# Optimization experiments

Hardware: AMD Instinct MI355X
Metric: run time of the kernel (lower is better)

The kernel has to match this reference:

```python
import jax, jax.numpy as jnp
import numpy as np

EMBED_DIM = 1024
N_TOKENS = 8192


def setup_inputs() -> dict:
    key = jax.random.key(0)
    k1, k2, k3 = jax.random.split(key, 3)
    inputs = jax.random.normal(k1, (N_TOKENS, EMBED_DIM), dtype=jnp.float32)
    rotation_params = jax.random.normal(k2, (EMBED_DIM, EMBED_DIM), dtype=jnp.float32)
    entangle_params = jax.random.normal(k3, (EMBED_DIM, EMBED_DIM), dtype=jnp.float32)
    return {"inputs": inputs, "rotation_params": rotation_params, "entangle_params": entangle_params}


def reference(inputs, rotation_params, entangle_params):
    # query/key projections from externally supplied params
    embed_dim = inputs.shape[-1]
    wq = rotation_params.reshape(embed_dim, -1)
    wk = entangle_params.reshape(embed_dim, -1)
    query = inputs @ wq          # [N, d]
    key = inputs @ wk            # [N, d]
    scale = 1.0 / jnp.sqrt(jnp.float32(embed_dim))
    scores = jax.nn.softmax(jnp.einsum('nd,md->nm', query, key) * scale, axis=-1)  # [N, N]
    context = scores @ inputs    # attend over raw inputs (V = inputs)
    return context
```

## Files before the change

kernel.cpp:

```cpp
#include <hip/hip_runtime.h>
#include <hip/hip_bf16.h>


typedef _Float16 f16x8 __attribute__((ext_vector_type(8)));
typedef float    f32x4 __attribute__((ext_vector_type(4)));

__device__ __forceinline__ void g2lds16(const _Float16* g, _Float16* l) {
    __builtin_amdgcn_global_load_lds(
        (__attribute__((address_space(1))) unsigned int*)(g),
        (__attribute__((address_space(3))) unsigned int*)(l),
        16, 0, 0);
}


__global__ void prep_x(const float* __restrict__ src,
                       _Float16* __restrict__ hi, _Float16* __restrict__ lo,
                       _Float16* __restrict__ xt, int R, int C) {
    __shared__ float tile[32][33];
    int c0 = blockIdx.x * 32, r0 = blockIdx.y * 32;
    int tx = threadIdx.x, ty = threadIdx.y;
#pragma unroll
    for (int k = 0; k < 4; ++k) {
        int r = ty + 8 * k;
        size_t idx = (size_t)(r0 + r) * C + c0 + tx;
        float v = src[idx];
        tile[r][tx] = v;
        _Float16 h = (_Float16)v;
        hi[idx] = h;
        lo[idx] = (_Float16)(v - (float)h);
    }
    __syncthreads();
#pragma unroll
    for (int k = 0; k < 4; ++k) {
        float v = tile[tx][ty + 8 * k];
        xt[(size_t)(c0 + ty + 8 * k) * R + r0 + tx] = (_Float16)v;
    }
}

__global__ void transpose_split(const float* __restrict__ src,
                                _Float16* __restrict__ dhi,
                                _Float16* __restrict__ dlo,
                                int R, int C) {
    __shared__ float tile[32][33];
    int c0 = blockIdx.x * 32, r0 = blockIdx.y * 32;
    int tx = threadIdx.x, ty = threadIdx.y;
#pragma unroll
    for (int k = 0; k < 4; ++k)
        tile[ty + 8 * k][tx] = src[(size_t)(r0 + ty + 8 * k) * C + c0 + tx];
    __syncthreads();
#pragma unroll
    for (int k = 0; k < 4; ++k) {
        float v = tile[tx][ty + 8 * k];
        _Float16 h = (_Float16)v;
        size_t idx = (size_t)(c0 + ty + 8 * k) * R + r0 + tx;
        dhi[idx] = h;
        dlo[idx] = (_Float16)(v - (float)h);
    }
}

__global__ __launch_bounds__(256) void add_rows(const float* __restrict__ a,
                                                const float* __restrict__ b,
                                                float* __restrict__ out, long n4) {
    long i = (long)blockIdx.x * blockDim.x + threadIdx.x;
    long stride = (long)gridDim.x * blockDim.x;
    for (; i < n4; i += stride) {
        float4 x = ((const float4*)a)[i];
        float4 y = ((const float4*)b)[i];
        x.x += y.x; x.y += y.y; x.z += y.z; x.w += y.w;
        ((float4*)out)[i] = x;
    }
}

template <int TERMS, int BKH, int SWAP, int SPLIT_OUT>
__global__ __launch_bounds__(512, 2) void gemm_p4(
    const _Float16* __restrict__ Ahi, const _Float16* __restrict__ Alo,
    const _Float16* __restrict__ Bhi, const _Float16* __restrict__ Blo,
    float* __restrict__ C, _Float16* __restrict__ Chi, _Float16* __restrict__ Clo,
    long lda, long ldb, long ldc, int K, int nrb, int ncb,
    long zA, long zB, long zC) {
    static_assert(BKH == 32 || BKH == 64, "");
    constexpr int NMAT = (TERMS == 3) ? 4 : 2;
    constexpr int KK   = BKH / 32;
    constexpr int LPR  = BKH / 8;
    constexpr int RPI  = 512 / LPR;
    constexpr int IPM  = 256 / RPI;
    constexpr int MATH = 256 * BKH;
    __shared__ __align__(16) _Float16 s[2][NMAT * MATH];

    const long z = blockIdx.z;
    Ahi += z * zA; Bhi += z * zB;
    if constexpr (TERMS == 3) { Alo += z * zA; Blo += z * zB; }
    if constexpr (SPLIT_OUT) { Chi += z * zC; Clo += z * zC; }
    else C += z * zC;

    const int nb = nrb * ncb;
    const int orig = blockIdx.x;
    const int q = nb >> 3, r8 = nb & 7;
    const int xcd = orig & 7, pos = orig >> 3;
    const int sw = (xcd < r8 ? xcd * (q + 1) : r8 * (q + 1) + (xcd - r8) * q) + pos;
    int rb, cb;
    if constexpr (SWAP) { rb = sw / ncb; cb = sw % ncb; }
    else                { cb = sw / nrb; rb = sw % nrb; }
    const long rowBase = (long)rb * 256;
    const long colBase = (long)cb * 256;

    const int t = threadIdx.x;
    const int wave = t >> 6;
    const int lane = t & 63;
    const int lm = lane & 15;
    const int lq = lane >> 4;
    const int wr = wave >> 2;
    const int wc = wave & 3;

    const int row0 = t / LPR;
    const int slot = t % LPR;
    const int swzW = (BKH == 32) ? ((row0 >> 1) & 3) : (row0 & 7);
    const _Float16* gsrc[NMAT];
    long gld[NMAT];
    gsrc[0] = Ahi + (rowBase + row0) * lda + (slot ^ swzW) * 8; gld[0] = lda;
    if constexpr (TERMS == 3) {
        gsrc[1] = Alo + (rowBase + row0) * lda + (slot ^ swzW) * 8; gld[1] = lda;
        gsrc[2] = Bhi + (colBase + row0) * ldb + (slot ^ swzW) * 8; gld[2] = ldb;
        gsrc[3] = Blo + (colBase + row0) * ldb + (slot ^ swzW) * 8; gld[3] = ldb;
    } else {
        gsrc[1] = Bhi + (colBase + row0) * ldb + (slot ^ swzW) * 8; gld[1] = ldb;
    }
    const int ldsRow = wave * (64 / LPR);

    const int swzR = (BKH == 32) ? ((lm >> 1) & 3) : (lm & 7);

    f32x4 acc[8][4];
#pragma unroll
    for (int rr = 0; rr < 8; ++rr)
#pragma unroll
        for (int cc = 0; cc < 4; ++cc)
#pragma unroll
            for (int i = 0; i < 4; ++i) acc[rr][cc][i] = 0.0f;

    const int NT = K / BKH;
    int cur = 0;

#pragma unroll
    for (int m = 0; m < NMAT; ++m)
#pragma unroll
        for (int j = 0; j < IPM; ++j)
            g2lds16(gsrc[m] + (long)(j * RPI) * gld[m],
                    &s[0][m * MATH + (j * RPI + ldsRow) * BKH]);
    __syncthreads();

    for (int tt = 0; tt < NT; ++tt) {
        const _Float16* sAh = &s[cur][0];
        const _Float16* sAl = sAh + MATH;
        const _Float16* sBh = sAh + (TERMS == 3 ? 2 : 1) * MATH;
        const _Float16* sBl = sAh + 3 * MATH;
        f16x8 bh[4 * KK], bl[TERMS == 3 ? 4 * KK : 1];
#pragma unroll
        for (int p = 0; p < 4; ++p) {
            if (p == 0 && tt + 1 < NT) {
                const long k0 = (long)(tt + 1) * BKH;
#pragma unroll
                for (int m = 0; m < NMAT; ++m)
#pragma unroll
                    for (int j = 0; j < IPM; ++j)
                        g2lds16(gsrc[m] + (long)(j * RPI) * gld[m] + k0,
                                &s[cur ^ 1][m * MATH + (j * RPI + ldsRow) * BKH]);
            }
            f16x8 ah[2 * KK], al[TERMS == 3 ? 2 * KK : 1];
#pragma unroll
            for (int rr = 0; rr < 2; ++rr) {
                const int arow = wr * 128 + (2 * p + rr) * 16 + lm;
#pragma unroll
                for (int kk = 0; kk < KK; ++kk) {
                    const int off = arow * BKH + (((kk * 4 + lq) ^ swzR) << 3);
                    ah[rr * KK + kk] = *(const f16x8*)&sAh[off];
                    if constexpr (TERMS == 3)
                        al[rr * KK + kk] = *(const f16x8*)&sAl[off];
                }
            }
            if (p == 0) {
#pragma unroll
                for (int cc = 0; cc < 4; ++cc) {
                    const int brow = wc * 64 + cc * 16 + lm;
#pragma unroll
                    for (int kk = 0; kk < KK; ++kk) {
                        const int off = brow * BKH + (((kk * 4 + lq) ^ swzR) << 3);
                        bh[cc * KK + kk] = *(const f16x8*)&sBh[off];
                        if constexpr (TERMS == 3)
                            bl[cc * KK + kk] = *(const f16x8*)&sBl[off];
                    }
                }
            }
            __builtin_amdgcn_s_barrier();
            asm volatile("s_waitcnt lgkmcnt(0)" ::: "memory");
            __builtin_amdgcn_sched_barrier(0);
            __builtin_amdgcn_s_setprio(1);
#pragma unroll
            for (int rr = 0; rr < 2; ++rr)
#pragma unroll
                for (int cc = 0; cc < 4; ++cc)
#pragma unroll
                    for (int kk = 0; kk < KK; ++kk) {
                        acc[2 * p + rr][cc] = __builtin_amdgcn_mfma_f32_16x16x32_f16(
                            ah[rr * KK + kk], bh[cc * KK + kk], acc[2 * p + rr][cc], 0, 0, 0);
                        if constexpr (TERMS == 3) {
                            acc[2 * p + rr][cc] = __builtin_amdgcn_mfma_f32_16x16x32_f16(
                                ah[rr * KK + kk], bl[cc * KK + kk], acc[2 * p + rr][cc], 0, 0, 0);
                            acc[2 * p + rr][cc] = __builtin_amdgcn_mfma_f32_16x16x32_f16(
                                al[rr * KK + kk], bh[cc * KK + kk], acc[2 * p + rr][cc], 0, 0, 0);
                        }
                    }
            __builtin_amdgcn_s_setprio(0);
            if (p < 3) __builtin_amdgcn_s_barrier();
        }
        __syncthreads();
        cur ^= 1;
    }

#pragma unroll
    for (int rr = 0; rr < 8; ++rr)
#pragma unroll
        for (int cc = 0; cc < 4; ++cc)
#pragma unroll
            for (int i = 0; i < 4; ++i) {
                const long row = rowBase + wr * 128 + rr * 16 + lq * 4 + i;
                const long col = colBase + wc * 64 + cc * 16 + lm;
                if constexpr (SPLIT_OUT) {
                    float v = acc[rr][cc][i];
                    _Float16 h = (_Float16)v;
                    Chi[row * ldc + col] = h;
                    Clo[row * ldc + col] = (_Float16)(v - (float)h);
                } else {
                    C[row * ldc + col] = acc[rr][cc][i];
                }
            }
}

__global__ __launch_bounds__(256) void softmax_rows(const float* __restrict__ S,
                                                    _Float16* __restrict__ P,
                                                    long ldp, int N) {
    const int row = blockIdx.x;
    const int t = threadIdx.x;
    const float4* rowp = (const float4*)(S + (size_t)row * N);
    float4 v[8];
    float mx = -3.4e38f;
#pragma unroll
    for (int g = 0; g < 4; ++g) {
        v[2 * g]     = rowp[2 * t + 512 * g];
        v[2 * g + 1] = rowp[2 * t + 512 * g + 1];
    }
#pragma unroll
    for (int i = 0; i < 8; ++i)
        mx = fmaxf(mx, fmaxf(fmaxf(v[i].x, v[i].y), fmaxf(v[i].z, v[i].w)));
    __shared__ float red[8];
#pragma unroll
    for (int off = 32; off >= 1; off >>= 1) mx = fmaxf(mx, __shfl_xor(mx, off));
    if ((t & 63) == 0) red[t >> 6] = mx;
    __syncthreads();
    mx = fmaxf(fmaxf(red[0], red[1]), fmaxf(red[2], red[3]));

    float sum = 0.0f;
#pragma unroll
    for (int i = 0; i < 8; ++i) {
        v[i].x = __expf((v[i].x - mx) * 0.03125f);
        v[i].y = __expf((v[i].y - mx) * 0.03125f);
        v[i].z = __expf((v[i].z - mx) * 0.03125f);
        v[i].w = __expf((v[i].w - mx) * 0.03125f);
        sum += (v[i].x + v[i].y) + (v[i].z + v[i].w);
    }
#pragma unroll
    for (int off = 32; off >= 1; off >>= 1) sum += __shfl_xor(sum, off);
    if ((t & 63) == 0) red[4 + (t >> 6)] = sum;
    __syncthreads();
    float inv = 1.0f / (red[4] + red[5] + red[6] + red[7]);

    f16x8* prow = (f16x8*)(P + (size_t)row * ldp);
#pragma unroll
    for (int g = 0; g < 4; ++g) {
        float4 a = v[2 * g], b = v[2 * g + 1];
        f16x8 o;
        o[0] = (_Float16)(a.x * inv); o[1] = (_Float16)(a.y * inv);
        o[2] = (_Float16)(a.z * inv); o[3] = (_Float16)(a.w * inv);
        o[4] = (_Float16)(b.x * inv); o[5] = (_Float16)(b.y * inv);
        o[6] = (_Float16)(b.z * inv); o[7] = (_Float16)(b.w * inv);
        prow[t + 256 * g] = o;
    }
}

extern "C" void kernel_launch(void* const* d_in, const int* in_sizes, int n_in,
                              void* d_out, int out_size, void* d_ws, size_t ws_size,
                              hipStream_t stream) {
    const float* X  = (const float*)d_in[0];
    const float* Wq = (const float*)d_in[1];
    const float* Wk = (const float*)d_in[2];
    float* out = (float*)d_out;

    const long Nt = 8192, D = 1024;
    char* ws = (char*)d_ws;
    const size_t MB = 1024ull * 1024ull;

    _Float16* XT  = (_Float16*)(ws + 0);
    _Float16* Qhi = (_Float16*)(ws + 16 * MB);
    _Float16* Qlo = (_Float16*)(ws + 32 * MB);
    _Float16* Khi = (_Float16*)(ws + 48 * MB);
    _Float16* Klo = (_Float16*)(ws + 64 * MB);
    _Float16* Xhi   = (_Float16*)(ws + 80 * MB);
    _Float16* Xlo   = (_Float16*)(ws + 96 * MB);
    _Float16* WqThi = (_Float16*)(ws + 112 * MB);
    _Float16* WqTlo = (_Float16*)(ws + 114 * MB);
    _Float16* WkThi = (_Float16*)(ws + 116 * MB);
    _Float16* WkTlo = (_Float16*)(ws + 118 * MB);
    float* PK0 = (float*)(ws + 16 * MB);

    const size_t rowBytes = (size_t)Nt * 4;
    const bool planA = ws_size >= 208 * MB + 256 * rowBytes;
    _Float16* Pbuf = (_Float16*)(ws + 80 * MB);
    float* Sc;
    long chunk;
    if (planA) {
        Sc = (float*)(ws + 208 * MB);
        size_t avail = ws_size - 208 * MB;
        chunk = (long)((avail / rowBytes / 256) * 256);
    } else {
        Sc = (float*)(ws + 80 * MB);
        size_t avail = ws_size > 80 * MB ? ws_size - 80 * MB : 0;
        chunk = (long)((avail / rowBytes / 256) * 256);
        if (chunk < 256) chunk = 256;
    }
    if (chunk > Nt) chunk = Nt;
    {
        long nch = (Nt + chunk - 1) / chunk;
        chunk = (((Nt + nch - 1) / nch) + 255) / 256 * 256;
    }

    prep_x<<<dim3(32, 256), dim3(32, 8), 0, stream>>>(X, Xhi, Xlo, XT,
                                                      (int)Nt, (int)D);
    transpose_split<<<dim3(32, 32), dim3(32, 8), 0, stream>>>(Wq, WqThi, WqTlo,
                                                              (int)D, (int)D);
    transpose_split<<<dim3(32, 32), dim3(32, 8), 0, stream>>>(Wk, WkThi, WkTlo,
                                                              (int)D, (int)D);

    gemm_p4<3, 32, 1, 1><<<dim3(32 * 4, 1, 2), 512, 0, stream>>>(
        Xhi, Xlo, WqThi, WqTlo, nullptr, Qhi, Qlo,
        D, D, D, (int)D, 32, 4,
        0, (long)(4 * MB / 2), (long)(32 * MB / 2));

    long done = 0;
    while (done < Nt) {
        long cur = Nt - done < chunk ? Nt - done : chunk;
        int nrb = (int)(cur / 256), ncb = (int)(Nt / 256);
        gemm_p4<3, 32, 1, 0><<<dim3(nrb * ncb, 1, 1), 512, 0, stream>>>(
            Qhi + done * D, Qlo + done * D, Khi, Klo, Sc, nullptr, nullptr,
            D, D, Nt, (int)D, nrb, ncb, 0, 0, 0);
        if (planA) {
            softmax_rows<<<(int)cur, 256, 0, stream>>>(Sc, Pbuf + done * Nt,
                                                       Nt, (int)Nt);
        } else {
            softmax_rows<<<(int)cur, 256, 0, stream>>>(Sc, (_Float16*)Sc,
                                                       2 * Nt, (int)Nt);
            gemm_p4<1, 64, 0, 0><<<dim3((int)(cur / 256) * 4, 1, 1), 512, 0, stream>>>(
                (const _Float16*)Sc, nullptr, XT, nullptr,
                out + done * D, nullptr, nullptr,
                2 * Nt, Nt, D, (int)Nt, (int)(cur / 256), 4, 0, 0, 0);
        }
        done += cur;
    }

    if (planA) {
        gemm_p4<1, 64, 0, 0><<<dim3(32 * 4, 1, 2), 512, 0, stream>>>(
            Pbuf, nullptr, XT, nullptr, PK0, nullptr, nullptr,
            Nt, Nt, D, (int)(Nt / 2), 32, 4,
            Nt / 2, Nt / 2, Nt * D);
        add_rows<<<1024, 256, 0, stream>>>(PK0, PK0 + Nt * D, out, Nt * D / 4);
    }
}
```

Baseline: 877.4 us.

## Stage GEMM tile loads per sub-phase with fine-grained vmcnt waits

Reassigns the global-to-LDS loads so each wave fetches the rows it later consumes, and spreads the next tile's prefetch across the four compute sub-phases. Fine-grained s_waitcnt vmcnt counts replace the per-tile __syncthreads, so each phase waits only for its own data, with a barrier at the end of every phase. This aims to overlap memory traffic with MFMA work and remove a full-block sync. The P@V GEMM launches also switch to row-major block swizzle ordering. The hand-counted vmcnt values are fragile: a wrong count could race on LDS.

New measurement: 822.0 us. 6.3% less time.

```diff
diff --git a/kernel.cpp b/kernel.cpp
--- a/kernel.cpp
+++ b/kernel.cpp
@@ -82,8 +82,6 @@
     constexpr int NMAT = (TERMS == 3) ? 4 : 2;
     constexpr int KK   = BKH / 32;
     constexpr int LPR  = BKH / 8;
-    constexpr int RPI  = 512 / LPR;
-    constexpr int IPM  = 256 / RPI;
     constexpr int MATH = 256 * BKH;
     __shared__ __align__(16) _Float16 s[2][NMAT * MATH];
 
@@ -111,21 +109,41 @@
     const int lq = lane >> 4;
     const int wr = wave >> 2;
     const int wc = wave & 3;
-
-    const int row0 = t / LPR;
-    const int slot = t % LPR;
-    const int swzW = (BKH == 32) ? ((row0 >> 1) & 3) : (row0 & 7);
-    const _Float16* gsrc[NMAT];
-    long gld[NMAT];
-    gsrc[0] = Ahi + (rowBase + row0) * lda + (slot ^ swzW) * 8; gld[0] = lda;
-    if constexpr (TERMS == 3) {
-        gsrc[1] = Alo + (rowBase + row0) * lda + (slot ^ swzW) * 8; gld[1] = lda;
-        gsrc[2] = Bhi + (colBase + row0) * ldb + (slot ^ swzW) * 8; gld[2] = ldb;
-        gsrc[3] = Blo + (colBase + row0) * ldb + (slot ^ swzW) * 8; gld[3] = ldb;
-    } else {
-        gsrc[1] = Bhi + (colBase + row0) * ldb + (slot ^ swzW) * 8; gld[1] = ldb;
-    }
-    const int ldsRow = wave * (64 / LPR);
+    const int wg = wave & 3;
+
+    const int ri   = lane / LPR;
+    const int slot = lane % LPR;
+    const int swzW = (BKH == 32) ? ((ri >> 1) & 3) : (ri & 7);
+    const int colOff = (slot ^ swzW) * 8;
+
+    const _Float16* gB[4]; int lB[4];
+    const _Float16* gA[4]; int lA[4];
+#pragma unroll
+    for (int b = 0; b < 4; ++b) {
+        if constexpr (TERMS == 3) {
+            const int rowW = (b >> 1) * 128 + wave * 16;
+            const _Float16* m = (b & 1) ? Blo : Bhi;
+            gB[b] = m + (colBase + rowW + ri) * ldb + colOff;
+            lB[b] = (2 + (b & 1)) * MATH + rowW * BKH;
+        } else {
+            const int rowW = b * 64 + wave * 8;
+            gB[b] = Bhi + (colBase + rowW + ri) * ldb + colOff;
+            lB[b] = MATH + rowW * BKH;
+        }
+    }
+#pragma unroll
+    for (int a = 0; a < 4; ++a) {
+        if constexpr (TERMS == 3) {
+            const int rowW = wr * 128 + (a >> 1) * 64 + wg * 16;
+            const _Float16* m = (a & 1) ? Alo : Ahi;
+            gA[a] = m + (rowBase + rowW + ri) * lda + colOff;
+            lA[a] = (a & 1) * MATH + rowW * BKH;
+        } else {
+            const int rowW = wr * 128 + a * 32 + wg * 8;
+            gA[a] = Ahi + (rowBase + rowW + ri) * lda + colOff;
+            lA[a] = rowW * BKH;
+        }
+    }
 
     const int swzR = (BKH == 32) ? ((lm >> 1) & 3) : (lm & 7);
 
@@ -138,17 +156,21 @@
             for (int i = 0; i < 4; ++i) acc[rr][cc][i] = 0.0f;
 
     const int NT = K / BKH;
+
+#define VMW(N) asm volatile("s_waitcnt vmcnt(" #N ")" ::: "memory")
+#define STB(b, buf, k0) g2lds16(gB[b] + (k0), &s[buf][lB[b]])
+#define STA(a, buf, k0) g2lds16(gA[a] + (k0), &s[buf][lA[a]])
+
+    STB(0, 0, 0); STB(1, 0, 0); STB(2, 0, 0); STB(3, 0, 0);
+    STA(0, 0, 0); STA(1, 0, 0); STA(2, 0, 0); STA(3, 0, 0);
+    if constexpr (TERMS == 3) { VMW(2); } else { VMW(3); }
+    __builtin_amdgcn_s_barrier();
+
     int cur = 0;
-
-#pragma unroll
-    for (int m = 0; m < NMAT; ++m)
-#pragma unroll
-        for (int j = 0; j < IPM; ++j)
-            g2lds16(gsrc[m] + (long)(j * RPI) * gld[m],
-                    &s[0][m * MATH + (j * RPI + ldsRow) * BKH]);
-    __syncthreads();
-
     for (int tt = 0; tt < NT; ++tt) {
+        const int nxt = cur ^ 1;
+        const bool nl = (tt + 1 < NT);
+        const long k1 = (long)(tt + 1) * BKH;
         const _Float16* sAh = &s[cur][0];
         const _Float16* sAl = sAh + MATH;
         const _Float16* sBh = sAh + (TERMS == 3 ? 2 : 1) * MATH;
@@ -156,15 +178,6 @@
         f16x8 bh[4 * KK], bl[TERMS == 3 ? 4 * KK : 1];
 #pragma unroll
         for (int p = 0; p < 4; ++p) {
-            if (p == 0 && tt + 1 < NT) {
-                const long k0 = (long)(tt + 1) * BKH;
-#pragma unroll
-                for (int m = 0; m < NMAT; ++m)
-#pragma unroll
-                    for (int j = 0; j < IPM; ++j)
-                        g2lds16(gsrc[m] + (long)(j * RPI) * gld[m] + k0,
-                                &s[cur ^ 1][m * MATH + (j * RPI + ldsRow) * BKH]);
-            }
             f16x8 ah[2 * KK], al[TERMS == 3 ? 2 * KK : 1];
 #pragma unroll
             for (int rr = 0; rr < 2; ++rr) {
@@ -189,6 +202,22 @@
                             bl[cc * KK + kk] = *(const f16x8*)&sBl[off];
                     }
                 }
+            }
+            if (nl) {
+                if (p == 0)      { STB(0, nxt, k1); STB(1, nxt, k1);
+                                   STB(2, nxt, k1); STB(3, nxt, k1); }
+                else if (p == 1) { STA(0, nxt, k1); STA(1, nxt, k1); }
+                else if (p == 2) { STA(2, nxt, k1); }
+                else             { STA(3, nxt, k1); }
+            }
+            if constexpr (TERMS == 3) {
+                if (p == 1)      { if (nl) { VMW(5); } else { VMW(0); } }
+                else if (p == 3) { if (nl) { VMW(2); } }
+            } else {
+                if (p == 0)      { if (nl) { VMW(6); } else { VMW(2); } }
+                else if (p == 1) { if (nl) { VMW(6); } else { VMW(1); } }
+                else if (p == 2) { if (nl) { VMW(7); } else { VMW(0); } }
+                else             { if (nl) { VMW(3); } }
             }
             __builtin_amdgcn_s_barrier();
             asm volatile("s_waitcnt lgkmcnt(0)" ::: "memory");
@@ -210,11 +239,13 @@
                         }
                     }
             __builtin_amdgcn_s_setprio(0);
-            if (p < 3) __builtin_amdgcn_s_barrier();
+            __builtin_amdgcn_s_barrier();
         }
-        __syncthreads();
-        cur ^= 1;
-    }
+        cur = nxt;
+    }
+#undef VMW
+#undef STB
+#undef STA
 
 #pragma unroll
     for (int rr = 0; rr < 8; ++rr)
@@ -357,7 +388,7 @@
         } else {
             softmax_rows<<<(int)cur, 256, 0, stream>>>(Sc, (_Float16*)Sc,
                                                        2 * Nt, (int)Nt);
-            gemm_p4<1, 64, 0, 0><<<dim3((int)(cur / 256) * 4, 1, 1), 512, 0, stream>>>(
+            gemm_p4<1, 64, 1, 0><<<dim3((int)(cur / 256) * 4, 1, 1), 512, 0, stream>>>(
                 (const _Float16*)Sc, nullptr, XT, nullptr,
                 out + done * D, nullptr, nullptr,
                 2 * Nt, Nt, D, (int)Nt, (int)(cur / 256), 4, 0, 0, 0);
@@ -366,7 +397,7 @@
     }
 
     if (planA) {
-        gemm_p4<1, 64, 0, 0><<<dim3(32 * 4, 1, 2), 512, 0, stream>>>(
+        gemm_p4<1, 64, 1, 0><<<dim3(32 * 4, 1, 2), 512, 0, stream>>>(
             Pbuf, nullptr, XT, nullptr, PK0, nullptr, nullptr,
             Nt, Nt, D, (int)(Nt / 2), 32, 4,
             Nt / 2, Nt / 2, Nt * D);
```
